# Performance work log

Measured on AMD Instinct MI355X. Metric: run time of the kernel, lower is better.

## Reference

```python
import jax, jax.numpy as jnp
import numpy as np

B, L, D = 4, 8192, 512
H, G = 8, 4
DH = D // H      # head channels = 64
GC = D // G      # group channels = 128
KSZ = 5          # kernel = offset_range_factor
PAD = KSZ // 2   # = 2; applied to BOTH offset convs (second conv has k=1, pad=2 -> length L+4)


def conv1d(x, w, b, pad):
    # x: (N, Cin, L), w: (Cout, Cin, K) torch layout
    y = jax.lax.conv_general_dilated(x, w, (1,), [(pad, pad)],
                                     dimension_numbers=('NCH', 'OIH', 'NCH'))
    return y + b[None, :, None]


def setup_inputs() -> dict:
    key = jax.random.key(0)
    ks = jax.random.split(key, 9)
    s = 0.02
    p = lambda k, shape: jax.random.normal(k, shape, jnp.float32) * s
    return {
        'x': jax.random.normal(ks[0], (B, L, D), jnp.float32),
        'Wq': p(ks[1], (D, D)), 'bq': jnp.zeros((D,), jnp.float32),
        'Wk': p(ks[2], (D, D)), 'bk': jnp.zeros((D,), jnp.float32),
        'Wv': p(ks[3], (D, D)), 'bv': jnp.zeros((D,), jnp.float32),
        'Woff1': p(ks[4], (GC, GC, KSZ)), 'boff1': jnp.zeros((GC,), jnp.float32),
        'Woff2': p(ks[5], (1, GC, 1)), 'boff2': jnp.zeros((1,), jnp.float32),
        'rel_bias': p(ks[6], (1, D, L)),
        'Wout': p(ks[7], (D, D)), 'bout': jnp.zeros((D,), jnp.float32),
    }


def reference(x, Wq, bq, Wk, bk, Wv, bv, Woff1, boff1, Woff2, boff2, rel_bias, Wout, bout):
    Bv, Lv, Dv = x.shape
    xc = jnp.transpose(x, (0, 2, 1))                         # (B, D, L)
    # 1x1 convs == pointwise linear over channels
    q = jnp.einsum('od,bdl->bol', Wq, xc) + bq[None, :, None]
    # offset prediction on grouped queries
    gq = q.reshape(Bv * G, GC, Lv)                            # (BG, GC, L)
    o = conv1d(gq, Woff1, boff1, PAD)                         # (BG, GC, L)
    o = conv1d(o, Woff2, boff2, PAD)                          # (BG, 1, L+4) due to k=1,pad=2
    offset = jnp.tanh(o[:, 0, :]) * KSZ                       # (BG, L+4)
    n = offset.shape[-1]
    vgrid = jnp.arange(n, dtype=x.dtype) + offset             # (BG, L+4)
    g = 2.0 * vgrid / (n - 1) - 1.0                           # normalized to [-1, 1] over n
    # torch grid_sample, align_corners=False, padding_mode='zeros', H = L
    pos = ((g + 1.0) * Lv - 1.0) / 2.0
    p0 = jnp.floor(pos)
    w1 = pos - p0                                             # weight for upper neighbor
    p0i = p0.astype(jnp.int32)
    p1i = p0i + 1
    feats = xc.reshape(Bv * G, GC, Lv)

    def gather(idx):
        valid = ((idx >= 0) & (idx < Lv)).astype(x.dtype)      # (BG, n)
        idxc = jnp.clip(idx, 0, Lv - 1)
        vals = jnp.take_along_axis(feats, idxc[:, None, :].astype(jnp.int32).repeat(1, axis=1), axis=2) if False else jnp.take_along_axis(feats, jnp.broadcast_to(idxc[:, None, :], (Bv * G, GC, n)), axis=2)
        return vals * valid[:, None, :]

    samp = gather(p0i) * (1.0 - w1)[:, None, :] + gather(p1i) * w1[:, None, :]
    x_sampled = samp[:, :, :Lv].reshape(Bv, Dv, Lv)           # (B, D, L)
    k = jnp.einsum('od,bdl->bol', Wk, x_sampled) + bk[None, :, None]
    v = jnp.einsum('od,bdl->bol', Wv, x_sampled) + bv[None, :, None] + rel_bias
    qh = q.reshape(Bv * H, DH, Lv)
    kh = k.reshape(Bv * H, DH, Lv)
    vh = v.reshape(Bv * H, DH, Lv)
    # channel-attention: contraction over sequence length L
    scores = jnp.einsum('bil,bjl->bij', qh, kh) * (Dv ** -0.5)  # (B*H, DH, DH)
    attn = jax.nn.softmax(scores, axis=-1)
    out = jnp.einsum('bij,bjl->bil', attn, vh)                # (B*H, DH, L)
    # rearrange '(b g) l c -> b c (g l)' with b=B, g=H, l=DH, c=L -> (B, L, D)
    out = jnp.transpose(out.reshape(Bv, H, DH, Lv), (0, 3, 1, 2)).reshape(Bv, Lv, H * DH)
    return out @ Wout.T + bout
```

## Files before the change

### kernel.cpp

```cpp
#include <hip/hip_runtime.h>
#include <hip/hip_bf16.h>
#include <math.h>

using u16 = unsigned short;
using u32 = unsigned int;

typedef __attribute__((ext_vector_type(8))) short s16x8;
typedef __attribute__((ext_vector_type(4))) float f32x4;

#define B_  4
#define L_  8192
#define D_  512
#define H_  8
#define G_  4

__device__ __forceinline__ float bf2f(u16 u) {
    u32 x = ((u32)u) << 16;
    return __uint_as_float(x);
}
__device__ __forceinline__ u16 f2bf(float f) {
    u32 x = __float_as_uint(f);
    u32 lsb = (x >> 16) & 1u;
    x += 0x7FFFu + lsb;
    return (u16)(x >> 16);
}
__device__ __forceinline__ void async16(const void* g, void* l) {
    __builtin_amdgcn_global_load_lds((const __attribute__((address_space(1))) u32*)g,
                                     (__attribute__((address_space(3))) u32*)l, 16, 0, 0);
}

__global__ __launch_bounds__(256) void cast_f32_bf16(const float* __restrict__ src,
                                                     u16* __restrict__ dst, int n4) {
    int i = blockIdx.x * 256 + threadIdx.x;
    if (i >= n4) return;
    float4 v = ((const float4*)src)[i];
    ushort4 o;
    o.x = f2bf(v.x); o.y = f2bf(v.y); o.z = f2bf(v.z); o.w = f2bf(v.w);
    ((ushort4*)dst)[i] = o;
}

__global__ __launch_bounds__(128) void build_weff(const float* __restrict__ W1,
                                                  const float* __restrict__ b1,
                                                  const float* __restrict__ W2,
                                                  const float* __restrict__ b2,
                                                  float* __restrict__ weff) {
    int idx = blockIdx.x * 128 + threadIdx.x;
    if (idx < 640) {
        int cin = idx / 5, dk = idx % 5;
        float acc = 0.f;
        for (int c = 0; c < 128; ++c) acc += W2[c] * W1[(c * 128 + cin) * 5 + dk];
        weff[idx] = acc;
    } else if (idx == 640) {
        float s = b2[0];
        for (int c = 0; c < 128; ++c) s += W2[c] * b1[c];
        weff[640] = s;
    } else if (idx == 641) {
        weff[641] = b2[0];
    }
}

__global__ __launch_bounds__(256) void offsets_kernel(const u16* __restrict__ qT,
                                                      const float* __restrict__ weff,
                                                      int* __restrict__ p0o,
                                                      float* __restrict__ w1o) {
    __shared__ u16 qs[128 * 72];
    __shared__ float wf[642];
    __shared__ float red[4][64];
    const int tid = threadIdx.x;
    const int t0 = blockIdx.x * 64;
    const int bg = blockIdx.y;
    const int b = bg >> 2, g = bg & 3;
    for (int i = tid; i < 642; i += 256) wf[i] = weff[i];
    for (int i = tid; i < 128 * 9; i += 256) {
        const int ch = i / 9, seg = i - ch * 9;
        const int l = t0 - 8 + seg * 8;
        s16x8 val = {0, 0, 0, 0, 0, 0, 0, 0};
        if (l >= 0)
            val = *(const s16x8*)(qT + (size_t)(b * D_ + g * 128 + ch) * L_ + l);
        *(s16x8*)(qs + ch * 72 + seg * 8) = val;
    }
    __syncthreads();
    const int w = tid >> 6, lane = tid & 63;
    float acc = 0.f;
    for (int c = 0; c < 32; ++c) {
        const int ch = w * 32 + c;
        const u16* row = qs + ch * 72 + lane + 4;
        const float* wr = wf + ch * 5;
        #pragma unroll
        for (int dk = 0; dk < 5; ++dk) acc += wr[dk] * bf2f(row[dk]);
    }
    red[w][lane] = acc;
    __syncthreads();
    if (w == 0) {
        const float s = red[0][lane] + red[1][lane] + red[2][lane] + red[3][lane];
        const int t = t0 + lane;
        const float o2 = (t >= 2) ? (s + wf[640]) : wf[641];
        const double offv = tanh((double)o2) * 5.0;
        const double vg  = (double)t + offv;
        const double gg  = 2.0 * vg / 8195.0 - 1.0;
        const double pos = ((gg + 1.0) * 8192.0 - 1.0) * 0.5;
        const double p0d = floor(pos);
        p0o[(size_t)bg * L_ + t] = (int)p0d;
        w1o[(size_t)bg * L_ + t] = (float)(pos - p0d);
    }
}

__global__ __launch_bounds__(256) void sample_kernel(const float* __restrict__ x,
                                                     const int* __restrict__ p0i,
                                                     const float* __restrict__ w1f,
                                                     u16* __restrict__ xs) {
    const size_t idx4 = (size_t)blockIdx.x * 256 + threadIdx.x;
    const int d4 = (int)(idx4 & 127);
    const int t = (int)((idx4 >> 7) & 8191);
    const int b = (int)(idx4 >> 20);
    const int g = d4 >> 5;
    const size_t og = (size_t)(b * 4 + g) * L_ + t;
    const int p0 = p0i[og];
    const float w1 = w1f[og];
    const float w0 = 1.f - w1;
    const int p1 = p0 + 1;
    float4 v0 = {0.f, 0.f, 0.f, 0.f}, v1 = {0.f, 0.f, 0.f, 0.f};
    if (p0 >= 0 && p0 < L_) v0 = *(const float4*)(x + ((size_t)b * L_ + p0) * D_ + d4 * 4);
    if (p1 >= 0 && p1 < L_) v1 = *(const float4*)(x + ((size_t)b * L_ + p1) * D_ + d4 * 4);
    ushort4 o;
    o.x = f2bf(v0.x * w0 + v1.x * w1);
    o.y = f2bf(v0.y * w0 + v1.y * w1);
    o.z = f2bf(v0.z * w0 + v1.z * w1);
    o.w = f2bf(v0.w * w0 + v1.w * w1);
    ((ushort4*)xs)[idx4] = o;
}

template <int MODE>
__global__ __launch_bounds__(256) void gemm_kernel(const u16* __restrict__ A,
                                                   const u16* __restrict__ W,
                                                   const float* __restrict__ bias,
                                                   const float* __restrict__ rel,
                                                   void* __restrict__ out) {
    __shared__ short As[128 * 32];
    __shared__ short Bs[128 * 32];
    const int tid = threadIdx.x;
    const int wave = tid >> 6, lane = tid & 63;
    const int bid = blockIdx.x;
    const int xcd = bid & 7;
    const int kk_ = bid >> 3;
    const int r0 = (xcd * 32 + (kk_ >> 2)) * 128;
    const int c0 = (kk_ & 3) * 128;
    const u16* Wb = (MODE == 2) ? (W + (size_t)(r0 >> 13) * D_ * D_) : W;
    const int wm = (wave >> 1) * 64, wn = (wave & 1) * 64;
    const int srow = lane >> 2;
    const int gcb  = (lane & 3) ^ ((srow >> 1) & 3);
    const int scol = gcb * 8;

    f32x4 acc[4][4];
    #pragma unroll
    for (int mi = 0; mi < 4; ++mi)
        #pragma unroll
        for (int ni = 0; ni < 4; ++ni) acc[mi][ni] = (f32x4){0.f, 0.f, 0.f, 0.f};

    const int fm = lane & 15;
    const int sblk = ((lane >> 4) ^ ((fm >> 1) & 3)) * 8;

    for (int k0 = 0; k0 < D_; k0 += 32) {
        #pragma unroll
        for (int i = 0; i < 2; ++i) {
            const int rr = wave * 32 + i * 16 + srow;
            const u16* ga = A  + (size_t)(r0 + rr) * D_ + k0 + scol;
            const u16* gb = Wb + (size_t)(c0 + rr) * D_ + k0 + scol;
            async16(ga, &As[(wave * 32 + i * 16) * 32]);
            async16(gb, &Bs[(wave * 32 + i * 16) * 32]);
        }
        __syncthreads();
        s16x8 af[4], bfr[4];
        #pragma unroll
        for (int mi = 0; mi < 4; ++mi) af[mi]  = *(const s16x8*)(As + (wm + mi * 16 + fm) * 32 + sblk);
        #pragma unroll
        for (int ni = 0; ni < 4; ++ni) bfr[ni] = *(const s16x8*)(Bs + (wn + ni * 16 + fm) * 32 + sblk);
        #pragma unroll
        for (int mi = 0; mi < 4; ++mi)
            #pragma unroll
            for (int ni = 0; ni < 4; ++ni)
                acc[mi][ni] = __builtin_amdgcn_mfma_f32_16x16x32_bf16(af[mi], bfr[ni], acc[mi][ni], 0, 0, 0);
        __syncthreads();
    }
    const int fn = lane & 15;
    const int q4 = (lane >> 4) * 4;
    #pragma unroll
    for (int mi = 0; mi < 4; ++mi) {
        #pragma unroll
        for (int ni = 0; ni < 4; ++ni) {
            const int c = c0 + wn + ni * 16 + fn;
            const float bsum = bias[c];
            if (MODE == 0) {
                const int r_ = r0 + wm + mi * 16 + q4;
                const int bb = r_ >> 13;
                const int l  = r_ & (L_ - 1);
                ushort4 o;
                o.x = f2bf(acc[mi][ni][0] + bsum);
                o.y = f2bf(acc[mi][ni][1] + bsum);
                o.z = f2bf(acc[mi][ni][2] + bsum);
                o.w = f2bf(acc[mi][ni][3] + bsum);
                *(ushort4*)((u16*)out + (size_t)(bb * D_ + c) * L_ + l) = o;
            } else {
                #pragma unroll
                for (int rg = 0; rg < 4; ++rg) {
                    const int r = r0 + wm + mi * 16 + q4 + rg;
                    float v = acc[mi][ni][rg] + bsum;
                    if (MODE == 1) v += rel[(size_t)c * L_ + (r & (L_ - 1))];
                    if (MODE == 2) ((float*)out)[(size_t)r * D_ + c] = v;
                    else           ((u16*)out)[(size_t)r * D_ + c] = f2bf(v);
                }
            }
        }
    }
}

__global__ __launch_bounds__(256) void scores_partial(const u16* __restrict__ qT,
                                                      const u16* __restrict__ kT,
                                                      float* __restrict__ part) {
    __shared__ u16 qs[64 * 136];
    __shared__ u16 ks[64 * 136];
    const int chunk = blockIdx.x;
    const int bh = blockIdx.y;
    const int b = bh >> 3, h = bh & 7;
    const int tid = threadIdx.x;
    const int wave = tid >> 6, lane = tid & 63;
    const int wr = (wave >> 1) * 32;
    const int wc = (wave & 1) * 32;
    f32x4 acc[2][2];
    #pragma unroll
    for (int mi = 0; mi < 2; ++mi)
        #pragma unroll
        for (int ni = 0; ni < 2; ++ni) acc[mi][ni] = (f32x4){0.f, 0.f, 0.f, 0.f};
    const size_t base = (size_t)(b * D_ + h * 64) * L_;
    const int m = lane & 15, q = lane >> 4;
    for (int iter = 0; iter < 4; ++iter) {
        const int l0 = chunk * 512 + iter * 128;
        __syncthreads();
        for (int i = tid; i < 1024; i += 256) {
            const int lb = i & 15, ch = i >> 4;
            const size_t gidx = base + (size_t)ch * L_ + l0 + lb * 8;
            *(s16x8*)(qs + ch * 136 + lb * 8) = *(const s16x8*)(qT + gidx);
            *(s16x8*)(ks + ch * 136 + lb * 8) = *(const s16x8*)(kT + gidx);
        }
        __syncthreads();
        #pragma unroll
        for (int kst = 0; kst < 4; ++kst) {
            const int kk = kst * 32 + q * 8;
            s16x8 af[2], bfr[2];
            af[0]  = *(const s16x8*)(qs + (wr + m) * 136 + kk);
            af[1]  = *(const s16x8*)(qs + (wr + 16 + m) * 136 + kk);
            bfr[0] = *(const s16x8*)(ks + (wc + m) * 136 + kk);
            bfr[1] = *(const s16x8*)(ks + (wc + 16 + m) * 136 + kk);
            #pragma unroll
            for (int mi = 0; mi < 2; ++mi)
                #pragma unroll
                for (int ni = 0; ni < 2; ++ni)
                    acc[mi][ni] = __builtin_amdgcn_mfma_f32_16x16x32_bf16(af[mi], bfr[ni], acc[mi][ni], 0, 0, 0);
        }
    }
    float* dst = part + (size_t)(bh * 16 + chunk) * 4096;
    const int q4 = (lane >> 4) * 4;
    #pragma unroll
    for (int mi = 0; mi < 2; ++mi) {
        #pragma unroll
        for (int ni = 0; ni < 2; ++ni) {
            const int j = wc + ni * 16 + m;
            #pragma unroll
            for (int rg = 0; rg < 4; ++rg) {
                const int i = wr + mi * 16 + q4 + rg;
                dst[i * 64 + j] = acc[mi][ni][rg];
            }
        }
    }
}

__global__ __launch_bounds__(256) void softmax_kernel(const float* __restrict__ part,
                                                      float* __restrict__ attn) {
    const int tid = threadIdx.x;
    const int wave = tid >> 6, lane = tid & 63;
    const int row = blockIdx.x * 4 + wave;
    const int bh = row >> 6, i = row & 63;
    float s = 0.f;
    #pragma unroll
    for (int c = 0; c < 16; ++c) s += part[((size_t)(bh * 16 + c)) * 4096 + i * 64 + lane];
    s *= 0.04419417382415922f;
    float m = s;
    for (int off = 32; off > 0; off >>= 1) m = fmaxf(m, __shfl_xor(m, off));
    float e = expf(s - m);
    float sum = e;
    for (int off = 32; off > 0; off >>= 1) sum += __shfl_xor(sum, off);
    attn[(size_t)bh * 4096 + i * 64 + lane] = e / sum;
}

__global__ __launch_bounds__(256) void build_M(const float* __restrict__ Wout,
                                               const float* __restrict__ attn,
                                               u16* __restrict__ M) {
    const int idx = blockIdx.x * 256 + threadIdx.x;
    const int col = idx & 511;
    const int o = (idx >> 9) & 511;
    const int b = idx >> 18;
    const int h = col >> 6, j = col & 63;
    const float* wr = Wout + o * 512 + h * 64;
    const float* ar = attn + (size_t)(b * H_ + h) * 4096 + j;
    float s = 0.f;
    #pragma unroll 8
    for (int i = 0; i < 64; ++i) s += wr[i] * ar[i * 64];
    M[idx] = f2bf(s);
}

extern "C" void kernel_launch(void* const* d_in, const int* in_sizes, int n_in,
                              void* d_out, int out_size, void* d_ws, size_t ws_size,
                              hipStream_t stream) {
    const float* x    = (const float*)d_in[0];
    const float* Wq   = (const float*)d_in[1];
    const float* bq   = (const float*)d_in[2];
    const float* Wk   = (const float*)d_in[3];
    const float* bk   = (const float*)d_in[4];
    const float* Wv   = (const float*)d_in[5];
    const float* bv   = (const float*)d_in[6];
    const float* Wo1  = (const float*)d_in[7];
    const float* bo1  = (const float*)d_in[8];
    const float* Wo2  = (const float*)d_in[9];
    const float* bo2  = (const float*)d_in[10];
    const float* rel  = (const float*)d_in[11];
    const float* Wout = (const float*)d_in[12];
    const float* bout = (const float*)d_in[13];

    char* ws = (char*)d_ws;
    const size_t MB = 1024ull * 1024ull;
    u16*   x_bf  = (u16*)(ws);
    u16*   qT    = (u16*)(ws + 32 * MB);
    u16*   kT    = (u16*)(ws + 64 * MB);
    u16*   v_bf  = (u16*)(ws + 96 * MB);
    u16*   wq_bf = (u16*)(ws + 128 * MB);
    u16*   wk_bf = wq_bf + 262144;
    u16*   wv_bf = wk_bf + 262144;
    float* weff  = (float*)(ws + 130 * MB);
    int*   p0i   = (int*)(ws + 130 * MB + 65536);
    float* w1f   = (float*)((char*)p0i + 524288);
    float* part  = (float*)((char*)w1f + 524288);
    float* attn  = (float*)((char*)part + 8 * MB);
    u16*   M_bf  = (u16*)((char*)attn + 524288);

    cast_f32_bf16<<<16384, 256, 0, stream>>>(x, x_bf, 4194304);
    cast_f32_bf16<<<256, 256, 0, stream>>>(Wq, wq_bf, 65536);
    cast_f32_bf16<<<256, 256, 0, stream>>>(Wk, wk_bf, 65536);
    cast_f32_bf16<<<256, 256, 0, stream>>>(Wv, wv_bf, 65536);
    build_weff<<<6, 128, 0, stream>>>(Wo1, bo1, Wo2, bo2, weff);
    gemm_kernel<0><<<1024, 256, 0, stream>>>(x_bf, wq_bf, bq, nullptr, (void*)qT);
    offsets_kernel<<<dim3(128, 16), 256, 0, stream>>>(qT, weff, p0i, w1f);
    sample_kernel<<<16384, 256, 0, stream>>>(x, p0i, w1f, x_bf);
    gemm_kernel<0><<<1024, 256, 0, stream>>>(x_bf, wk_bf, bk, nullptr, (void*)kT);
    gemm_kernel<1><<<1024, 256, 0, stream>>>(x_bf, wv_bf, bv, rel, (void*)v_bf);
    scores_partial<<<dim3(16, 32), 256, 0, stream>>>(qT, kT, part);
    softmax_kernel<<<512, 256, 0, stream>>>(part, attn);
    build_M<<<4096, 256, 0, stream>>>(Wout, attn, M_bf);
    gemm_kernel<2><<<1024, 256, 0, stream>>>(v_bf, M_bf, bout, nullptr, d_out);
}
```

Measured before the change: 409.3 us.

## Double-buffer per-wave GEMM tiles with async LDS loads and manual waitcnt

Restructures the GEMM main loop so each wave loads only its own 64-row A and B slices into a private double-buffered LDS region. Explicit vmcnt/lgkmcnt waits replace the two block-wide barriers per k-step, letting the next tile's global loads overlap MFMA work. The MODE 1 epilogue also reads rel_bias as float4 instead of per-element scalar loads. Per-wave private tiles mean A and B are no longer shared across waves, so global and LDS traffic per block doubles. Correctness depends on the hand-coded waitcnt encodings.

```diff
diff --git a/kernel.cpp b/kernel.cpp
--- a/kernel.cpp
+++ b/kernel.cpp
@@ -28,6 +28,9 @@
     __builtin_amdgcn_global_load_lds((const __attribute__((address_space(1))) u32*)g,
                                      (__attribute__((address_space(3))) u32*)l, 16, 0, 0);
 }
+#define WAIT_VM8   0x0F78
+#define WAIT_VM0   0x0F70
+#define WAIT_LGKM0 0xC07F
 
 __global__ __launch_bounds__(256) void cast_f32_bf16(const float* __restrict__ src,
                                                      u16* __restrict__ dst, int n4) {
@@ -136,8 +139,7 @@
                                                    const float* __restrict__ bias,
                                                    const float* __restrict__ rel,
                                                    void* __restrict__ out) {
-    __shared__ short As[128 * 32];
-    __shared__ short Bs[128 * 32];
+    __shared__ short lds[4][2][4096];
     const int tid = threadIdx.x;
     const int wave = tid >> 6, lane = tid & 63;
     const int bid = blockIdx.x;
@@ -148,8 +150,12 @@
     const u16* Wb = (MODE == 2) ? (W + (size_t)(r0 >> 13) * D_ * D_) : W;
     const int wm = (wave >> 1) * 64, wn = (wave & 1) * 64;
     const int srow = lane >> 2;
-    const int gcb  = (lane & 3) ^ ((srow >> 1) & 3);
-    const int scol = gcb * 8;
+    const int scol = ((lane & 3) ^ ((srow >> 1) & 3)) * 8;
+
+    const u16* gA = A  + (size_t)(r0 + wm) * D_ + scol;
+    const u16* gB = Wb + (size_t)(c0 + wn) * D_ + scol;
+    short* bufA[2] = {&lds[wave][0][0],    &lds[wave][1][0]};
+    short* bufB[2] = {&lds[wave][0][2048], &lds[wave][1][2048]};
 
     f32x4 acc[4][4];
     #pragma unroll
@@ -158,30 +164,47 @@
         for (int ni = 0; ni < 4; ++ni) acc[mi][ni] = (f32x4){0.f, 0.f, 0.f, 0.f};
 
     const int fm = lane & 15;
-    const int sblk = ((lane >> 4) ^ ((fm >> 1) & 3)) * 8;
-
-    for (int k0 = 0; k0 < D_; k0 += 32) {
-        #pragma unroll
-        for (int i = 0; i < 2; ++i) {
-            const int rr = wave * 32 + i * 16 + srow;
-            const u16* ga = A  + (size_t)(r0 + rr) * D_ + k0 + scol;
-            const u16* gb = Wb + (size_t)(c0 + rr) * D_ + k0 + scol;
-            async16(ga, &As[(wave * 32 + i * 16) * 32]);
-            async16(gb, &Bs[(wave * 32 + i * 16) * 32]);
-        }
-        __syncthreads();
+    const int sblk = (((lane >> 4) ^ ((fm >> 1) & 3))) * 8;
+
+    auto issue = [&](int bf, int k0) {
+        #pragma unroll
+        for (int j = 0; j < 4; ++j) {
+            async16(gA + (size_t)(j * 16 + srow) * D_ + k0, bufA[bf] + j * 512);
+            async16(gB + (size_t)(j * 16 + srow) * D_ + k0, bufB[bf] + j * 512);
+        }
+    };
+    auto consume = [&](int bf) {
         s16x8 af[4], bfr[4];
         #pragma unroll
-        for (int mi = 0; mi < 4; ++mi) af[mi]  = *(const s16x8*)(As + (wm + mi * 16 + fm) * 32 + sblk);
-        #pragma unroll
-        for (int ni = 0; ni < 4; ++ni) bfr[ni] = *(const s16x8*)(Bs + (wn + ni * 16 + fm) * 32 + sblk);
+        for (int mi = 0; mi < 4; ++mi) af[mi]  = *(const s16x8*)(bufA[bf] + mi * 512 + fm * 32 + sblk);
+        #pragma unroll
+        for (int ni = 0; ni < 4; ++ni) bfr[ni] = *(const s16x8*)(bufB[bf] + ni * 512 + fm * 32 + sblk);
         #pragma unroll
         for (int mi = 0; mi < 4; ++mi)
             #pragma unroll
             for (int ni = 0; ni < 4; ++ni)
                 acc[mi][ni] = __builtin_amdgcn_mfma_f32_16x16x32_bf16(af[mi], bfr[ni], acc[mi][ni], 0, 0, 0);
-        __syncthreads();
-    }
+    };
+
+    issue(0, 0);
+    issue(1, 32);
+    int bf = 0;
+    for (int k0 = 0; k0 < D_ - 64; k0 += 32) {
+        __builtin_amdgcn_s_waitcnt(WAIT_VM8);
+        __builtin_amdgcn_sched_barrier(0);
+        consume(bf);
+        __builtin_amdgcn_sched_barrier(0);
+        __builtin_amdgcn_s_waitcnt(WAIT_LGKM0);
+        issue(bf, k0 + 64);
+        bf ^= 1;
+    }
+    __builtin_amdgcn_s_waitcnt(WAIT_VM8);
+    __builtin_amdgcn_sched_barrier(0);
+    consume(bf);
+    __builtin_amdgcn_s_waitcnt(WAIT_VM0);
+    __builtin_amdgcn_sched_barrier(0);
+    consume(bf ^ 1);
+
     const int fn = lane & 15;
     const int q4 = (lane >> 4) * 4;
     #pragma unroll
@@ -200,14 +223,19 @@
                 o.z = f2bf(acc[mi][ni][2] + bsum);
                 o.w = f2bf(acc[mi][ni][3] + bsum);
                 *(ushort4*)((u16*)out + (size_t)(bb * D_ + c) * L_ + l) = o;
+            } else if (MODE == 1) {
+                const int r_ = r0 + wm + mi * 16 + q4;
+                const int l  = r_ & (L_ - 1);
+                const float4 rl = *(const float4*)(rel + (size_t)c * L_ + l);
+                ((u16*)out)[(size_t)(r_ + 0) * D_ + c] = f2bf(acc[mi][ni][0] + bsum + rl.x);
+                ((u16*)out)[(size_t)(r_ + 1) * D_ + c] = f2bf(acc[mi][ni][1] + bsum + rl.y);
+                ((u16*)out)[(size_t)(r_ + 2) * D_ + c] = f2bf(acc[mi][ni][2] + bsum + rl.z);
+                ((u16*)out)[(size_t)(r_ + 3) * D_ + c] = f2bf(acc[mi][ni][3] + bsum + rl.w);
             } else {
                 #pragma unroll
                 for (int rg = 0; rg < 4; ++rg) {
                     const int r = r0 + wm + mi * 16 + q4 + rg;
-                    float v = acc[mi][ni][rg] + bsum;
-                    if (MODE == 1) v += rel[(size_t)c * L_ + (r & (L_ - 1))];
-                    if (MODE == 2) ((float*)out)[(size_t)r * D_ + c] = v;
-                    else           ((u16*)out)[(size_t)r * D_ + c] = f2bf(v);
+                    ((float*)out)[(size_t)r * D_ + c] = acc[mi][ni][rg] + bsum;
                 }
             }
         }
```

Measured after the change: 403.5 us. No clear change (-1.4%).

## Load GEMM MFMA fragments directly from global with register double-buffering

Applied to the files above, without the earlier changes.

The GEMM kernel no longer stages A and W tiles through LDS with async global-to-LDS loads and per-iteration barriers. Each wave now loads its MFMA operand fragments straight from global memory into registers, prefetching the next K slice while the current one is computed. The MODE 1 epilogue also reads the rel_bias values as one float4 per four rows instead of four scalar loads. The change removes LDS traffic and syncthreads, but global loads are redundant across the waves sharing a tile, register use grows, and the 16-byte row-strided loads may coalesce poorly.

```diff
diff --git a/kernel.cpp b/kernel.cpp
--- a/kernel.cpp
+++ b/kernel.cpp
@@ -23,10 +23,6 @@
     u32 lsb = (x >> 16) & 1u;
     x += 0x7FFFu + lsb;
     return (u16)(x >> 16);
-}
-__device__ __forceinline__ void async16(const void* g, void* l) {
-    __builtin_amdgcn_global_load_lds((const __attribute__((address_space(1))) u32*)g,
-                                     (__attribute__((address_space(3))) u32*)l, 16, 0, 0);
 }
 
 __global__ __launch_bounds__(256) void cast_f32_bf16(const float* __restrict__ src,
@@ -136,8 +132,6 @@
                                                    const float* __restrict__ bias,
                                                    const float* __restrict__ rel,
                                                    void* __restrict__ out) {
-    __shared__ short As[128 * 32];
-    __shared__ short Bs[128 * 32];
     const int tid = threadIdx.x;
     const int wave = tid >> 6, lane = tid & 63;
     const int bid = blockIdx.x;
@@ -147,9 +141,11 @@
     const int c0 = (kk_ & 3) * 128;
     const u16* Wb = (MODE == 2) ? (W + (size_t)(r0 >> 13) * D_ * D_) : W;
     const int wm = (wave >> 1) * 64, wn = (wave & 1) * 64;
-    const int srow = lane >> 2;
-    const int gcb  = (lane & 3) ^ ((srow >> 1) & 3);
-    const int scol = gcb * 8;
+    const int fm = lane & 15;
+    const int kq = (lane >> 4) * 8;
+
+    const u16* gA = A  + (size_t)(r0 + wm + fm) * D_ + kq;
+    const u16* gB = Wb + (size_t)(c0 + wn + fm) * D_ + kq;
 
     f32x4 acc[4][4];
     #pragma unroll
@@ -157,31 +153,29 @@
         #pragma unroll
         for (int ni = 0; ni < 4; ++ni) acc[mi][ni] = (f32x4){0.f, 0.f, 0.f, 0.f};
 
-    const int fm = lane & 15;
-    const int sblk = ((lane >> 4) ^ ((fm >> 1) & 3)) * 8;
-
-    for (int k0 = 0; k0 < D_; k0 += 32) {
-        #pragma unroll
-        for (int i = 0; i < 2; ++i) {
-            const int rr = wave * 32 + i * 16 + srow;
-            const u16* ga = A  + (size_t)(r0 + rr) * D_ + k0 + scol;
-            const u16* gb = Wb + (size_t)(c0 + rr) * D_ + k0 + scol;
-            async16(ga, &As[(wave * 32 + i * 16) * 32]);
-            async16(gb, &Bs[(wave * 32 + i * 16) * 32]);
-        }
-        __syncthreads();
-        s16x8 af[4], bfr[4];
-        #pragma unroll
-        for (int mi = 0; mi < 4; ++mi) af[mi]  = *(const s16x8*)(As + (wm + mi * 16 + fm) * 32 + sblk);
-        #pragma unroll
-        for (int ni = 0; ni < 4; ++ni) bfr[ni] = *(const s16x8*)(Bs + (wn + ni * 16 + fm) * 32 + sblk);
+    s16x8 a[2][4], b[2][4];
+    #pragma unroll
+    for (int mi = 0; mi < 4; ++mi) a[0][mi] = *(const s16x8*)(gA + mi * 16 * D_);
+    #pragma unroll
+    for (int ni = 0; ni < 4; ++ni) b[0][ni] = *(const s16x8*)(gB + ni * 16 * D_);
+
+    #pragma unroll
+    for (int it = 0; it < 16; ++it) {
+        const int cur = it & 1, nxt = cur ^ 1;
+        if (it < 15) {
+            const int k1 = (it + 1) * 32;
+            #pragma unroll
+            for (int mi = 0; mi < 4; ++mi) a[nxt][mi] = *(const s16x8*)(gA + mi * 16 * D_ + k1);
+            #pragma unroll
+            for (int ni = 0; ni < 4; ++ni) b[nxt][ni] = *(const s16x8*)(gB + ni * 16 * D_ + k1);
+        }
         #pragma unroll
         for (int mi = 0; mi < 4; ++mi)
             #pragma unroll
             for (int ni = 0; ni < 4; ++ni)
-                acc[mi][ni] = __builtin_amdgcn_mfma_f32_16x16x32_bf16(af[mi], bfr[ni], acc[mi][ni], 0, 0, 0);
-        __syncthreads();
-    }
+                acc[mi][ni] = __builtin_amdgcn_mfma_f32_16x16x32_bf16(a[cur][mi], b[cur][ni], acc[mi][ni], 0, 0, 0);
+    }
+
     const int fn = lane & 15;
     const int q4 = (lane >> 4) * 4;
     #pragma unroll
@@ -200,14 +194,19 @@
                 o.z = f2bf(acc[mi][ni][2] + bsum);
                 o.w = f2bf(acc[mi][ni][3] + bsum);
                 *(ushort4*)((u16*)out + (size_t)(bb * D_ + c) * L_ + l) = o;
+            } else if (MODE == 1) {
+                const int r_ = r0 + wm + mi * 16 + q4;
+                const int l  = r_ & (L_ - 1);
+                const float4 rl = *(const float4*)(rel + (size_t)c * L_ + l);
+                ((u16*)out)[(size_t)(r_ + 0) * D_ + c] = f2bf(acc[mi][ni][0] + bsum + rl.x);
+                ((u16*)out)[(size_t)(r_ + 1) * D_ + c] = f2bf(acc[mi][ni][1] + bsum + rl.y);
+                ((u16*)out)[(size_t)(r_ + 2) * D_ + c] = f2bf(acc[mi][ni][2] + bsum + rl.z);
+                ((u16*)out)[(size_t)(r_ + 3) * D_ + c] = f2bf(acc[mi][ni][3] + bsum + rl.w);
             } else {
                 #pragma unroll
                 for (int rg = 0; rg < 4; ++rg) {
                     const int r = r0 + wm + mi * 16 + q4 + rg;
-                    float v = acc[mi][ni][rg] + bsum;
-                    if (MODE == 1) v += rel[(size_t)c * L_ + (r & (L_ - 1))];
-                    if (MODE == 2) ((float*)out)[(size_t)r * D_ + c] = v;
-                    else           ((u16*)out)[(size_t)r * D_ + c] = f2bf(v);
+                    ((float*)out)[(size_t)r * D_ + c] = acc[mi][ni][rg] + bsum;
                 }
             }
         }
```

Result: slower. 537.9 us (+31.4%).
